# Kernel optimization log

Hardware: AMD Instinct MI355X
Metric: run time of the kernel (lower is better)

Reference implementation:

```python
import jax, jax.numpy as jnp
import numpy as np

EMB = 1024
HEAD = 64


def setup_inputs() -> dict:
    key = jax.random.key(0)
    kx, kq, kk, kv = jax.random.split(key, 4)
    x = jax.random.normal(kx, (4, 4096, EMB), dtype=jnp.float32)
    # nn.Linear(emb, head, bias=False): y = x @ W^T; store transposed [emb, head]
    s = 1.0 / np.sqrt(EMB)
    Wq = jax.random.uniform(kq, (EMB, HEAD), jnp.float32, -s, s)
    Wk = jax.random.uniform(kk, (EMB, HEAD), jnp.float32, -s, s)
    Wv = jax.random.uniform(kv, (EMB, HEAD), jnp.float32, -s, s)
    return {"x": x, "Wq": Wq, "Wk": Wk, "Wv": Wv}


def reference(x, Wq, Wk, Wv):
    # x: [B, T, E]; projections -> [B, T, H]
    Q = jnp.einsum("bte,eh->bth", x, Wq)
    K = jnp.einsum("bte,eh->bth", x, Wk)
    V = jnp.einsum("bte,eh->bth", x, Wv)
    scale = 1.0 / np.sqrt(HEAD).astype(np.float32)
    scores = jnp.einsum("bqh,bkh->bqk", Q, K) * scale  # [B, T, T]
    attn = jax.nn.softmax(scores, axis=-1)
    out = jnp.einsum("bqk,bkh->bqh", attn, V)  # [B, T, H]
    return out
```

## Files before the change

### kernel.cpp

```cpp
#include <hip/hip_runtime.h>
#include <hip/hip_bf16.h>

typedef __bf16 bf16x8 __attribute__((ext_vector_type(8)));
typedef float floatx4 __attribute__((ext_vector_type(4)));

#define B_ 4
#define T_ 4096
#define E_ 1024
#define H_ 64
#define NSEG 8
#define SEGLEN (T_ / NSEG)
#define NROWS (B_ * T_)

#define QSCALE 0.18033688011112042f

#if __has_builtin(__builtin_amdgcn_exp2f)
#define EXP2(x) __builtin_amdgcn_exp2f(x)
#else
#define EXP2(x) exp2f(x)
#endif

__device__ __forceinline__ floatx4 mfma16(bf16x8 a, bf16x8 b, floatx4 c) {
  return __builtin_amdgcn_mfma_f32_16x16x32_bf16(a, b, c, 0, 0, 0);
}

#define GLDS16(gp, lp)                                                        \
  __builtin_amdgcn_global_load_lds(                                           \
      (const __attribute__((address_space(1))) void*)(gp),                    \
      (__attribute__((address_space(3))) void*)(lp), 16, 0, 0)

#define WAITCNT_VM(n) asm volatile("s_waitcnt vmcnt(" #n ")" ::: "memory")

__global__ void prep_wt_k(const float* __restrict__ Wq, const float* __restrict__ Wk,
                          const float* __restrict__ Wv, __bf16* __restrict__ Wfrag) {
  int gid = blockIdx.x * 4 + (threadIdx.x >> 6);
  int lane = threadIdx.x & 63;
  int ch = gid / 24, rem = gid % 24;
  int nt = rem >> 1, half = rem & 1;
  int g = lane >> 4, lm = lane & 15;
  int w = nt >> 2;
  const float* W = (w == 0) ? Wq : (w == 1) ? Wk : Wv;
  float sc = (w == 0) ? QSCALE : 1.0f;
  int h = (nt & 3) * 16 + lm;
  int e0 = ch * 64 + half * 32 + g * 8;
  __bf16* dst = Wfrag + (size_t)gid * 1024 / 2 + lane * 8;
  bf16x8 v;
#pragma unroll
  for (int j = 0; j < 8; j++) v[j] = (__bf16)(W[(size_t)(e0 + j) * H_ + h] * sc);
  *(bf16x8*)dst = v;
}

__global__ __launch_bounds__(256, 2) void proj_k(
    const float* __restrict__ x, const __bf16* __restrict__ Wfrag,
    __bf16* __restrict__ Qo, __bf16* __restrict__ Ko, __bf16* __restrict__ Vt) {
  __shared__ __align__(16) char sX[4 * 8192];

  int tid = threadIdx.x;
  int wv = tid >> 6, lane = tid & 63;
  int lm = lane & 15, g = lane >> 4;
  int row_base = blockIdx.x * 32;

  const char* xb = (const char*)x;
  const char* wfb = (const char*)Wfrag + (size_t)(wv * 3 * 2) * 1024 + lane * 16;

  int xrow[2], xswz[2];
#pragma unroll
  for (int i = 0; i < 2; i++) {
    int s = i * 256 + tid;
    xrow[i] = s >> 4;
    xswz[i] = ((s & 15) ^ (xrow[i] & 15)) << 4;
  }

#define STAGE_X(buf, ch)                                                      \
  _Pragma("unroll") for (int i = 0; i < 2; i++)                               \
      GLDS16(xb + (size_t)(row_base + xrow[i]) * 4096 + (size_t)(ch) * 256 +  \
                 xswz[i],                                                     \
             sX + (buf) * 8192 + (i * 256 + tid) * 16);

  bf16x8 wreg[2][6];
#define LOAD_W(set, ch)                                                       \
  _Pragma("unroll") for (int j = 0; j < 6; j++)                               \
      wreg[set][j] = *(const bf16x8*)(wfb + ((size_t)(ch) * 24 + j) * 1024);

  floatx4 acc[2][3];
#pragma unroll
  for (int rg = 0; rg < 2; rg++)
#pragma unroll
    for (int i = 0; i < 3; i++) acc[rg][i] = (floatx4)0.0f;

  STAGE_X(0, 0);
  LOAD_W(0, 0);
  __builtin_amdgcn_sched_barrier(0);
  STAGE_X(1, 1);
  LOAD_W(1, 1);

#pragma unroll
  for (int ch = 0; ch < 16; ch++) {
    if (ch < 15) {
      WAITCNT_VM(8);
    } else {
      WAITCNT_VM(0);
    }
    __builtin_amdgcn_sched_barrier(0);
    __builtin_amdgcn_s_barrier();
    __builtin_amdgcn_sched_barrier(0);

    if (ch < 14) STAGE_X((ch + 2) & 3, ch + 2);

    const char* xB = sX + (ch & 3) * 8192;
    bf16x8 a[2][2];
#pragma unroll
    for (int rg = 0; rg < 2; rg++)
#pragma unroll
      for (int ks = 0; ks < 2; ks++) {
        int c0 = ks * 8 + g * 2;
        const char* xp = xB + (rg * 16 + lm) * 256;
        float4 f0 = *(const float4*)(xp + ((c0 ^ lm) << 4));
        float4 f1 = *(const float4*)(xp + (((c0 + 1) ^ lm) << 4));
        a[rg][ks][0] = (__bf16)f0.x; a[rg][ks][1] = (__bf16)f0.y;
        a[rg][ks][2] = (__bf16)f0.z; a[rg][ks][3] = (__bf16)f0.w;
        a[rg][ks][4] = (__bf16)f1.x; a[rg][ks][5] = (__bf16)f1.y;
        a[rg][ks][6] = (__bf16)f1.z; a[rg][ks][7] = (__bf16)f1.w;
      }
#pragma unroll
    for (int i = 0; i < 3; i++) {
      bf16x8 b0 = wreg[ch & 1][i * 2];
      bf16x8 b1 = wreg[ch & 1][i * 2 + 1];
#pragma unroll
      for (int rg = 0; rg < 2; rg++) {
        acc[rg][i] = mfma16(a[rg][0], b0, acc[rg][i]);
        acc[rg][i] = mfma16(a[rg][1], b1, acc[rg][i]);
      }
    }

    if (ch < 14) LOAD_W(ch & 1, ch + 2);
  }

#pragma unroll
  for (int i = 0; i < 3; i++) {
    int nt = wv * 3 + i;
    int w = nt >> 2;
    int h = (nt & 3) * 16 + lm;
#pragma unroll
    for (int rg = 0; rg < 2; rg++)
#pragma unroll
      for (int r = 0; r < 4; r++) {
        __bf16 v = (__bf16)acc[rg][i][r];
        int rr = row_base + rg * 16 + g * 4 + r;
        if (w == 0)      Qo[(size_t)rr * H_ + h] = v;
        else if (w == 1) Ko[(size_t)rr * H_ + h] = v;
        else {
          int b = rr >> 12, t = rr & (T_ - 1);
          int kin = t & 63;
          int pos = ((kin >> 5) << 5) + (((kin >> 2) & 3) << 3) +
                    (((kin >> 4) & 1) << 2) + (kin & 3);
          Vt[((size_t)b * H_ + h) * T_ + (t & ~63) + pos] = v;
        }
      }
  }
}

__global__ __launch_bounds__(256, 2) void attn_k(
    const __bf16* __restrict__ Q, const __bf16* __restrict__ K,
    const __bf16* __restrict__ Vt, __bf16* __restrict__ Op, float* __restrict__ lp) {
  __shared__ __align__(16) char sK[2 * 8192];
  __shared__ __align__(16) char sV[2 * 8192];

  int qb = blockIdx.x, b = blockIdx.y, seg = blockIdx.z;
  int tid = threadIdx.x, wv = tid >> 6, lane = tid & 63;
  int lm = lane & 15, g = lane >> 4;
  int q0 = qb * 256 + wv * 64;

  const __bf16* Qb = Q + (size_t)b * T_ * H_;
  const char* Kb = (const char*)(K + (size_t)b * T_ * H_);
  const char* Vb = (const char*)(Vt + (size_t)b * H_ * T_);

  bf16x8 qf[4][2];
#pragma unroll
  for (int qi = 0; qi < 4; qi++)
#pragma unroll
    for (int hs = 0; hs < 2; hs++)
      qf[qi][hs] =
          *(const bf16x8*)&Qb[(size_t)(q0 + qi * 16 + lm) * H_ + hs * 32 + g * 8];

  floatx4 o_acc[4][4], o_l[4];
#pragma unroll
  for (int qi = 0; qi < 4; qi++) {
#pragma unroll
    for (int i = 0; i < 4; i++) o_acc[qi][i] = (floatx4)0.0f;
    o_l[qi] = (floatx4)0.0f;
  }

  bf16x8 vone;
#pragma unroll
  for (int j = 0; j < 8; j++) vone[j] = (__bf16)1.0f;

  int s3 = lm & 7;
  int koff[4][2], voff[2][4];
#pragma unroll
  for (int mt = 0; mt < 4; mt++) {
    koff[mt][0] = (mt * 16 + lm) * 128 + ((g ^ s3) << 4);
    koff[mt][1] = (mt * 16 + lm) * 128 + (((g + 4) ^ s3) << 4);
  }
#pragma unroll
  for (int ks = 0; ks < 2; ks++)
#pragma unroll
    for (int nt = 0; nt < 4; nt++)
      voff[ks][nt] = (nt * 16 + lm) * 128 + (((ks * 4 + g) ^ s3) << 4);

  int srow = tid >> 3, schk = tid & 7;
  int swz0 = (schk ^ (srow & 7)) << 4;

#define ATTN_STAGE(buf, k0_)                                                  \
  {                                                                           \
    int off = (buf) * 8192 + tid * 16;                                        \
    GLDS16(Kb + (size_t)(k0_ + srow) * 128 + swz0, sK + off);                 \
    GLDS16(Kb + (size_t)(k0_ + srow + 32) * 128 + swz0, sK + off + 4096);     \
    GLDS16(Vb + (size_t)srow * (T_ * 2) + (size_t)(k0_) * 2 + swz0, sV + off);\
    GLDS16(Vb + (size_t)(srow + 32) * (T_ * 2) + (size_t)(k0_) * 2 + swz0,    \
           sV + off + 4096);                                                  \
  }

  int kbase = seg * SEGLEN;
  ATTN_STAGE(0, kbase);
  __syncthreads();

  for (int t = 0; t < SEGLEN / 64; t++) {
    if (t + 1 < SEGLEN / 64) ATTN_STAGE((t + 1) & 1, kbase + (t + 1) * 64);
    const char* kB = sK + (t & 1) * 8192;
    const char* vB = sV + (t & 1) * 8192;

    floatx4 s_acc[4][4];
#pragma unroll
    for (int mt = 0; mt < 4; mt++)
#pragma unroll
      for (int qi = 0; qi < 4; qi++) s_acc[mt][qi] = (floatx4)0.0f;
#pragma unroll
    for (int mt = 0; mt < 4; mt++) {
      bf16x8 a0 = *(const bf16x8*)(kB + koff[mt][0]);
      bf16x8 a1 = *(const bf16x8*)(kB + koff[mt][1]);
#pragma unroll
      for (int qi = 0; qi < 4; qi++) {
        s_acc[mt][qi] = mfma16(a0, qf[qi][0], s_acc[mt][qi]);
        s_acc[mt][qi] = mfma16(a1, qf[qi][1], s_acc[mt][qi]);
      }
    }

    bf16x8 pa[4][2];
#pragma unroll
    for (int qi = 0; qi < 4; qi++)
#pragma unroll
      for (int mt = 0; mt < 4; mt++)
#pragma unroll
        for (int r = 0; r < 4; r++)
          pa[qi][mt >> 1][(mt & 1) * 4 + r] = (__bf16)EXP2(s_acc[mt][qi][r]);

#pragma unroll
    for (int ks = 0; ks < 2; ks++) {
      bf16x8 bb[4];
#pragma unroll
      for (int nt = 0; nt < 4; nt++) bb[nt] = *(const bf16x8*)(vB + voff[ks][nt]);
#pragma unroll
      for (int qi = 0; qi < 4; qi++) {
#pragma unroll
        for (int nt = 0; nt < 4; nt++)
          o_acc[qi][nt] = mfma16(pa[qi][ks], bb[nt], o_acc[qi][nt]);
        o_l[qi] = mfma16(pa[qi][ks], vone, o_l[qi]);
      }
    }
    __syncthreads();
  }

  size_t rowbase = (size_t)seg * NROWS + (size_t)b * T_ + qb * 256 + wv * 64;
#pragma unroll
  for (int qi = 0; qi < 4; qi++) {
#pragma unroll
    for (int nt = 0; nt < 4; nt++)
#pragma unroll
      for (int r = 0; r < 4; r++)
        Op[(rowbase + qi * 16 + g * 4 + r) * 64 + nt * 16 + lm] =
            (__bf16)o_acc[qi][nt][r];
    if (lm == 0) {
#pragma unroll
      for (int r = 0; r < 4; r++)
        lp[rowbase + qi * 16 + g * 4 + r] = o_l[qi][r];
    }
  }
}

__global__ void combine_k(const __bf16* __restrict__ Op, const float* __restrict__ lp,
                          float* __restrict__ out) {
  int base = (blockIdx.x * 256 + threadIdx.x) * 8;
  int row = base >> 6;
  float L = 0.0f;
  float o[8];
#pragma unroll
  for (int j = 0; j < 8; j++) o[j] = 0.0f;
#pragma unroll
  for (int s = 0; s < NSEG; s++) {
    L += lp[(size_t)s * NROWS + row];
    bf16x8 v = *(const bf16x8*)&Op[(size_t)s * NROWS * 64 + base];
#pragma unroll
    for (int j = 0; j < 8; j++) o[j] += (float)v[j];
  }
  float inv = 1.0f / L;
  float4 r0 = {o[0] * inv, o[1] * inv, o[2] * inv, o[3] * inv};
  float4 r1 = {o[4] * inv, o[5] * inv, o[6] * inv, o[7] * inv};
  *(float4*)&out[base] = r0;
  *(float4*)&out[base + 4] = r1;
}

extern "C" void kernel_launch(void* const* d_in, const int* in_sizes, int n_in,
                              void* d_out, int out_size, void* d_ws, size_t ws_size,
                              hipStream_t stream) {
  const float* x  = (const float*)d_in[0];
  const float* Wq = (const float*)d_in[1];
  const float* Wk = (const float*)d_in[2];
  const float* Wv = (const float*)d_in[3];
  float* out = (float*)d_out;

  char* ws = (char*)d_ws;
  __bf16* Wf  = (__bf16*)(ws);
  __bf16* Qs  = (__bf16*)(ws + 0x60000);
  __bf16* Ks  = (__bf16*)(ws + 0x260000);
  __bf16* Vts = (__bf16*)(ws + 0x460000);
  __bf16* Op  = (__bf16*)(ws + 0x660000);
  float*  lp  = (float*)(ws + 0x1660000);

  prep_wt_k<<<96, 256, 0, stream>>>(Wq, Wk, Wv, Wf);
  proj_k<<<NROWS / 32, 256, 0, stream>>>(x, Wf, Qs, Ks, Vts);
  attn_k<<<dim3(T_ / 256, B_, NSEG), 256, 0, stream>>>(Qs, Ks, Vts, Op, lp);
  combine_k<<<NROWS * 64 / (256 * 8), 256, 0, stream>>>(Op, lp, out);
}
```

Baseline: 53.41 us.

## Restructure projection kernel to single-wave blocks of 16 rows without barriers

The QKV projection kernel becomes one 64-lane wave per block that handles 16 rows and all 12 output tiles. It stages x into a private LDS ring and waits only on its own vmcnt, so no block-level barriers are needed. Weight fragments are now loaded directly from global/L2 each chunk instead of being double-buffered in registers. This removes inter-wave synchronisation and allows many more small blocks, at the cost of more weight traffic per row and higher register pressure from 12 accumulators.

```diff
diff --git a/kernel.cpp b/kernel.cpp
--- a/kernel.cpp
+++ b/kernel.cpp
@@ -50,113 +50,108 @@
   *(bf16x8*)dst = v;
 }
 
-__global__ __launch_bounds__(256, 2) void proj_k(
+__global__ __launch_bounds__(64) void proj_k(
     const float* __restrict__ x, const __bf16* __restrict__ Wfrag,
     __bf16* __restrict__ Qo, __bf16* __restrict__ Ko, __bf16* __restrict__ Vt) {
-  __shared__ __align__(16) char sX[4 * 8192];
-
-  int tid = threadIdx.x;
-  int wv = tid >> 6, lane = tid & 63;
+  __shared__ __align__(16) char sX[4 * 4096];
+
+  int lane = threadIdx.x;
   int lm = lane & 15, g = lane >> 4;
-  int row_base = blockIdx.x * 32;
+  int row_base = blockIdx.x * 16;
 
   const char* xb = (const char*)x;
-  const char* wfb = (const char*)Wfrag + (size_t)(wv * 3 * 2) * 1024 + lane * 16;
-
-  int xrow[2], xswz[2];
-#pragma unroll
-  for (int i = 0; i < 2; i++) {
-    int s = i * 256 + tid;
-    xrow[i] = s >> 4;
-    xswz[i] = ((s & 15) ^ (xrow[i] & 15)) << 4;
-  }
+  const char* wfb = (const char*)Wfrag + lane * 16;
+
+  int srow = lane >> 4, sc = lane & 15;
 
 #define STAGE_X(buf, ch)                                                      \
-  _Pragma("unroll") for (int i = 0; i < 2; i++)                               \
-      GLDS16(xb + (size_t)(row_base + xrow[i]) * 4096 + (size_t)(ch) * 256 +  \
-                 xswz[i],                                                     \
-             sX + (buf) * 8192 + (i * 256 + tid) * 16);
-
-  bf16x8 wreg[2][6];
-#define LOAD_W(set, ch)                                                       \
-  _Pragma("unroll") for (int j = 0; j < 6; j++)                               \
-      wreg[set][j] = *(const bf16x8*)(wfb + ((size_t)(ch) * 24 + j) * 1024);
-
-  floatx4 acc[2][3];
-#pragma unroll
-  for (int rg = 0; rg < 2; rg++)
-#pragma unroll
-    for (int i = 0; i < 3; i++) acc[rg][i] = (floatx4)0.0f;
+  _Pragma("unroll") for (int i = 0; i < 4; i++) {                             \
+    int r = i * 4 + srow;                                                     \
+    GLDS16(xb + (size_t)(row_base + r) * 4096 + (size_t)(ch) * 256 +          \
+               ((sc ^ r) << 4),                                               \
+           sX + (buf) * 4096 + i * 1024 + lane * 16);                         \
+  }
+
+  int aoff[2][2];
+#pragma unroll
+  for (int ks = 0; ks < 2; ks++) {
+    int c0 = ks * 8 + g * 2;
+    aoff[ks][0] = lm * 256 + ((c0 ^ lm) << 4);
+    aoff[ks][1] = lm * 256 + (((c0 + 1) ^ lm) << 4);
+  }
+
+  floatx4 acc[12];
+#pragma unroll
+  for (int i = 0; i < 12; i++) acc[i] = (floatx4)0.0f;
 
   STAGE_X(0, 0);
-  LOAD_W(0, 0);
-  __builtin_amdgcn_sched_barrier(0);
   STAGE_X(1, 1);
-  LOAD_W(1, 1);
 
 #pragma unroll
   for (int ch = 0; ch < 16; ch++) {
-    if (ch < 15) {
+    __builtin_amdgcn_sched_barrier(0);
+    if (ch < 14) STAGE_X((ch + 2) & 3, ch + 2);
+    __builtin_amdgcn_sched_barrier(0);
+    if (ch < 14) {
       WAITCNT_VM(8);
+    } else if (ch == 14) {
+      WAITCNT_VM(4);
     } else {
       WAITCNT_VM(0);
     }
     __builtin_amdgcn_sched_barrier(0);
-    __builtin_amdgcn_s_barrier();
-    __builtin_amdgcn_sched_barrier(0);
-
-    if (ch < 14) STAGE_X((ch + 2) & 3, ch + 2);
-
-    const char* xB = sX + (ch & 3) * 8192;
-    bf16x8 a[2][2];
-#pragma unroll
-    for (int rg = 0; rg < 2; rg++)
-#pragma unroll
-      for (int ks = 0; ks < 2; ks++) {
-        int c0 = ks * 8 + g * 2;
-        const char* xp = xB + (rg * 16 + lm) * 256;
-        float4 f0 = *(const float4*)(xp + ((c0 ^ lm) << 4));
-        float4 f1 = *(const float4*)(xp + (((c0 + 1) ^ lm) << 4));
-        a[rg][ks][0] = (__bf16)f0.x; a[rg][ks][1] = (__bf16)f0.y;
-        a[rg][ks][2] = (__bf16)f0.z; a[rg][ks][3] = (__bf16)f0.w;
-        a[rg][ks][4] = (__bf16)f1.x; a[rg][ks][5] = (__bf16)f1.y;
-        a[rg][ks][6] = (__bf16)f1.z; a[rg][ks][7] = (__bf16)f1.w;
-      }
-#pragma unroll
-    for (int i = 0; i < 3; i++) {
-      bf16x8 b0 = wreg[ch & 1][i * 2];
-      bf16x8 b1 = wreg[ch & 1][i * 2 + 1];
-#pragma unroll
-      for (int rg = 0; rg < 2; rg++) {
-        acc[rg][i] = mfma16(a[rg][0], b0, acc[rg][i]);
-        acc[rg][i] = mfma16(a[rg][1], b1, acc[rg][i]);
-      }
-    }
-
-    if (ch < 14) LOAD_W(ch & 1, ch + 2);
-  }
-
-#pragma unroll
-  for (int i = 0; i < 3; i++) {
-    int nt = wv * 3 + i;
+
+    const char* xB = sX + (ch & 3) * 4096;
+    bf16x8 a[2];
+#pragma unroll
+    for (int ks = 0; ks < 2; ks++) {
+      float4 f0 = *(const float4*)(xB + aoff[ks][0]);
+      float4 f1 = *(const float4*)(xB + aoff[ks][1]);
+      a[ks][0] = (__bf16)f0.x; a[ks][1] = (__bf16)f0.y;
+      a[ks][2] = (__bf16)f0.z; a[ks][3] = (__bf16)f0.w;
+      a[ks][4] = (__bf16)f1.x; a[ks][5] = (__bf16)f1.y;
+      a[ks][6] = (__bf16)f1.z; a[ks][7] = (__bf16)f1.w;
+    }
+
+    const char* wp = wfb + (size_t)ch * 24576;
+    bf16x8 wA[6], wB[6];
+#pragma unroll
+    for (int j = 0; j < 6; j++) wA[j] = *(const bf16x8*)(wp + (size_t)j * 2048);
+#pragma unroll
+    for (int j = 0; j < 6; j++) wB[j] = *(const bf16x8*)(wp + (size_t)(6 + j) * 2048);
+#pragma unroll
+    for (int j = 0; j < 6; j++) acc[j] = mfma16(a[0], wA[j], acc[j]);
+#pragma unroll
+    for (int j = 0; j < 6; j++) wA[j] = *(const bf16x8*)(wp + (size_t)j * 2048 + 1024);
+#pragma unroll
+    for (int j = 0; j < 6; j++) acc[6 + j] = mfma16(a[0], wB[j], acc[6 + j]);
+#pragma unroll
+    for (int j = 0; j < 6; j++)
+      wB[j] = *(const bf16x8*)(wp + (size_t)(6 + j) * 2048 + 1024);
+#pragma unroll
+    for (int j = 0; j < 6; j++) acc[j] = mfma16(a[1], wA[j], acc[j]);
+#pragma unroll
+    for (int j = 0; j < 6; j++) acc[6 + j] = mfma16(a[1], wB[j], acc[6 + j]);
+  }
+
+#pragma unroll
+  for (int nt = 0; nt < 12; nt++) {
     int w = nt >> 2;
     int h = (nt & 3) * 16 + lm;
 #pragma unroll
-    for (int rg = 0; rg < 2; rg++)
-#pragma unroll
-      for (int r = 0; r < 4; r++) {
-        __bf16 v = (__bf16)acc[rg][i][r];
-        int rr = row_base + rg * 16 + g * 4 + r;
-        if (w == 0)      Qo[(size_t)rr * H_ + h] = v;
-        else if (w == 1) Ko[(size_t)rr * H_ + h] = v;
-        else {
-          int b = rr >> 12, t = rr & (T_ - 1);
-          int kin = t & 63;
-          int pos = ((kin >> 5) << 5) + (((kin >> 2) & 3) << 3) +
-                    (((kin >> 4) & 1) << 2) + (kin & 3);
-          Vt[((size_t)b * H_ + h) * T_ + (t & ~63) + pos] = v;
-        }
+    for (int r = 0; r < 4; r++) {
+      __bf16 v = (__bf16)acc[nt][r];
+      int rr = row_base + g * 4 + r;
+      if (w == 0)      Qo[(size_t)rr * H_ + h] = v;
+      else if (w == 1) Ko[(size_t)rr * H_ + h] = v;
+      else {
+        int b = rr >> 12, t = rr & (T_ - 1);
+        int kin = t & 63;
+        int pos = ((kin >> 5) << 5) + (((kin >> 2) & 3) << 3) +
+                  (((kin >> 4) & 1) << 2) + (kin & 3);
+        Vt[((size_t)b * H_ + h) * T_ + (t & ~63) + pos] = v;
       }
+    }
   }
 }
 
@@ -328,7 +323,7 @@
   float*  lp  = (float*)(ws + 0x1660000);
 
   prep_wt_k<<<96, 256, 0, stream>>>(Wq, Wk, Wv, Wf);
-  proj_k<<<NROWS / 32, 256, 0, stream>>>(x, Wf, Qs, Ks, Vts);
+  proj_k<<<NROWS / 16, 64, 0, stream>>>(x, Wf, Qs, Ks, Vts);
   attn_k<<<dim3(T_ / 256, B_, NSEG), 256, 0, stream>>>(Qs, Ks, Vts, Op, lp);
   combine_k<<<NROWS * 64 / (256 * 8), 256, 0, stream>>>(Op, lp, out);
 }
```

Result: slower. 66.63 us (+24.8%).

## Replace pipelined projection loop with single-buffer LDS staging of x and weights

Applied to the files above, without the earlier changes.

The projection kernel drops its four-deep x ring buffer, register double-buffering of weight fragments, and manual vmcnt waits. Each chunk now loads x and the weight fragments into LDS with global_load_lds, synchronizes, computes, and synchronizes again. This simplifies the code and shares weight loads through LDS, but removes the overlap of memory loads with MFMA work and adds two block barriers per iteration.

```diff
diff --git a/kernel.cpp b/kernel.cpp
--- a/kernel.cpp
+++ b/kernel.cpp
@@ -28,8 +28,6 @@
   __builtin_amdgcn_global_load_lds(                                           \
       (const __attribute__((address_space(1))) void*)(gp),                    \
       (__attribute__((address_space(3))) void*)(lp), 16, 0, 0)
-
-#define WAITCNT_VM(n) asm volatile("s_waitcnt vmcnt(" #n ")" ::: "memory")
 
 __global__ void prep_wt_k(const float* __restrict__ Wq, const float* __restrict__ Wk,
                           const float* __restrict__ Wv, __bf16* __restrict__ Wfrag) {
@@ -50,10 +48,11 @@
   *(bf16x8*)dst = v;
 }
 
-__global__ __launch_bounds__(256, 2) void proj_k(
+__global__ void proj_k(
     const float* __restrict__ x, const __bf16* __restrict__ Wfrag,
     __bf16* __restrict__ Qo, __bf16* __restrict__ Ko, __bf16* __restrict__ Vt) {
-  __shared__ __align__(16) char sX[4 * 8192];
+  __shared__ __align__(16) char sX[8192];
+  __shared__ __align__(16) char sW[24576];
 
   int tid = threadIdx.x;
   int wv = tid >> 6, lane = tid & 63;
@@ -61,7 +60,7 @@
   int row_base = blockIdx.x * 32;
 
   const char* xb = (const char*)x;
-  const char* wfb = (const char*)Wfrag + (size_t)(wv * 3 * 2) * 1024 + lane * 16;
+  const char* wfb = (const char*)Wfrag;
 
   int xrow[2], xswz[2];
 #pragma unroll
@@ -71,50 +70,30 @@
     xswz[i] = ((s & 15) ^ (xrow[i] & 15)) << 4;
   }
 
-#define STAGE_X(buf, ch)                                                      \
-  _Pragma("unroll") for (int i = 0; i < 2; i++)                               \
-      GLDS16(xb + (size_t)(row_base + xrow[i]) * 4096 + (size_t)(ch) * 256 +  \
-                 xswz[i],                                                     \
-             sX + (buf) * 8192 + (i * 256 + tid) * 16);
-
-  bf16x8 wreg[2][6];
-#define LOAD_W(set, ch)                                                       \
-  _Pragma("unroll") for (int j = 0; j < 6; j++)                               \
-      wreg[set][j] = *(const bf16x8*)(wfb + ((size_t)(ch) * 24 + j) * 1024);
-
   floatx4 acc[2][3];
 #pragma unroll
   for (int rg = 0; rg < 2; rg++)
 #pragma unroll
     for (int i = 0; i < 3; i++) acc[rg][i] = (floatx4)0.0f;
 
-  STAGE_X(0, 0);
-  LOAD_W(0, 0);
-  __builtin_amdgcn_sched_barrier(0);
-  STAGE_X(1, 1);
-  LOAD_W(1, 1);
-
-#pragma unroll
   for (int ch = 0; ch < 16; ch++) {
-    if (ch < 15) {
-      WAITCNT_VM(8);
-    } else {
-      WAITCNT_VM(0);
-    }
-    __builtin_amdgcn_sched_barrier(0);
-    __builtin_amdgcn_s_barrier();
-    __builtin_amdgcn_sched_barrier(0);
-
-    if (ch < 14) STAGE_X((ch + 2) & 3, ch + 2);
-
-    const char* xB = sX + (ch & 3) * 8192;
+#pragma unroll
+    for (int i = 0; i < 2; i++)
+      GLDS16(xb + (size_t)(row_base + xrow[i]) * 4096 + (size_t)ch * 256 + xswz[i],
+             sX + (i * 256 + tid) * 16);
+#pragma unroll
+    for (int j = 0; j < 6; j++)
+      GLDS16(wfb + (size_t)ch * 24576 + j * 4096 + tid * 16,
+             sW + j * 4096 + tid * 16);
+    __syncthreads();
+
     bf16x8 a[2][2];
 #pragma unroll
     for (int rg = 0; rg < 2; rg++)
 #pragma unroll
       for (int ks = 0; ks < 2; ks++) {
         int c0 = ks * 8 + g * 2;
-        const char* xp = xB + (rg * 16 + lm) * 256;
+        const char* xp = sX + (rg * 16 + lm) * 256;
         float4 f0 = *(const float4*)(xp + ((c0 ^ lm) << 4));
         float4 f1 = *(const float4*)(xp + (((c0 + 1) ^ lm) << 4));
         a[rg][ks][0] = (__bf16)f0.x; a[rg][ks][1] = (__bf16)f0.y;
@@ -122,18 +101,19 @@
         a[rg][ks][4] = (__bf16)f1.x; a[rg][ks][5] = (__bf16)f1.y;
         a[rg][ks][6] = (__bf16)f1.z; a[rg][ks][7] = (__bf16)f1.w;
       }
+
+    const char* wB = sW + (size_t)(wv * 3 * 2) * 1024 + lane * 16;
 #pragma unroll
     for (int i = 0; i < 3; i++) {
-      bf16x8 b0 = wreg[ch & 1][i * 2];
-      bf16x8 b1 = wreg[ch & 1][i * 2 + 1];
+      bf16x8 b0 = *(const bf16x8*)(wB + (size_t)(i * 2) * 1024);
+      bf16x8 b1 = *(const bf16x8*)(wB + (size_t)(i * 2 + 1) * 1024);
 #pragma unroll
       for (int rg = 0; rg < 2; rg++) {
         acc[rg][i] = mfma16(a[rg][0], b0, acc[rg][i]);
         acc[rg][i] = mfma16(a[rg][1], b1, acc[rg][i]);
       }
     }
-
-    if (ch < 14) LOAD_W(ch & 1, ch + 2);
+    __syncthreads();
   }
 
 #pragma unroll
```

Result: slower. 57.64 us (+7.9%).
